# Kernel tuning notes

Hardware: AMD Instinct MI355X
Metric: run time of the kernel (lower is better)

## Reference

```python
import jax, jax.numpy as jnp
import numpy as np

N_NODES = 100000
N_EDGES = 1600000
IN_F = 128
OUT_F = 32


def setup_inputs() -> dict:
    key = jax.random.key(0)
    k1, k2, k3 = jax.random.split(key, 3)
    x = jax.random.normal(k1, (N_NODES, IN_F), dtype=jnp.float32)
    edge_index = jax.random.randint(k2, (2, N_EDGES), 0, N_NODES, dtype=jnp.int64)
    W = jax.random.normal(k3, (OUT_F, IN_F), dtype=jnp.float32) * 0.1
    b = jnp.zeros((OUT_F,), dtype=jnp.float32)
    return {"x": x, "edge_index": edge_index, "W": W, "b": b}


def reference(x, edge_index, W, b):
    # PyG GCNConv: add self-loops, symmetric normalization, linear, aggregate, bias
    N = x.shape[0]
    loops = jnp.arange(N, dtype=edge_index.dtype)
    src = jnp.concatenate([edge_index[0], loops])  # message source j
    dst = jnp.concatenate([edge_index[1], loops])  # aggregation target i
    ones = jnp.ones(src.shape[0], dtype=x.dtype)
    deg = jax.ops.segment_sum(ones, dst, num_segments=N)  # deg computed at col (target)
    dis = jnp.where(deg > 0, jax.lax.rsqrt(deg), 0.0)  # deg^{-1/2}, inf -> 0
    norm = dis[src] * dis[dst]  # [E+N]
    h = x @ W.T  # [N, OUT_F] linear transform first (PyG order)
    msg = h[src] * norm[:, None]  # [E+N, OUT_F] gathered, normalized messages
    out = jax.ops.segment_sum(msg, dst, num_segments=N)  # scatter-add aggregate
    return out + b
```

## Files before the change

### kernel.cpp

```cpp
#include <hip/hip_runtime.h>

#define IN_F 128
#define OUT_F 32
#define BKT_SHIFT 9
#define BKT_NODES 512
#define NBKT 196
#define PART_CHUNK 4096
#define SORT_CAP 12288

typedef unsigned int uint32;

__device__ __forceinline__ float bf2f(uint32 u) {
    union { uint32 ui; float f; } c; c.ui = u << 16; return c.f;
}
__device__ __forceinline__ uint32 f2bf(float x) {
    union { float f; uint32 ui; } c; c.f = x;
    uint32 u = c.ui;
    u += 0x7fffu + ((u >> 16) & 1u);
    return u >> 16;
}

__global__ void __launch_bounds__(256) k_bhist(const int* __restrict__ dst,
                                               int* __restrict__ bcnt, int E) {
    __shared__ int h[256];
    int t = threadIdx.x;
    h[t] = 0;
    __syncthreads();
    int stride = gridDim.x * 256;
    for (int e = blockIdx.x * 256 + t; e < E; e += stride)
        atomicAdd(&h[dst[e] >> BKT_SHIFT], 1);
    __syncthreads();
    if (h[t]) atomicAdd(&bcnt[t], h[t]);
}

__global__ void __launch_bounds__(256) k_bscan(const int* __restrict__ bcnt,
        int* __restrict__ bbase, int* __restrict__ gcur, int nbkt) {
    __shared__ int sc[256];
    int t = threadIdx.x;
    int v0 = (t < nbkt) ? bcnt[t] + 1431655766 : 0;
    sc[t] = v0;
    __syncthreads();
    #pragma unroll
    for (int ofs = 1; ofs < 256; ofs <<= 1) {
        int v = sc[t];
        int u = (t >= ofs) ? sc[t - ofs] : 0;
        __syncthreads();
        sc[t] = v + u;
        __syncthreads();
    }
    int excl = t ? sc[t - 1] : 0;
    if (t < nbkt) { bbase[t] = excl; gcur[t] = excl; }
    if (t == 255) bbase[nbkt] = sc[255];
}

__global__ void __launch_bounds__(256) k_part(
        const int* __restrict__ src, const int* __restrict__ dst,
        int* __restrict__ gcur, uint32* __restrict__ pk, int E) {
    __shared__ int    hist[256];
    __shared__ int    sc[256];
    __shared__ int    cbase[256];
    __shared__ int    gbase[256];
    __shared__ uint32 stage[PART_CHUNK];
    int t = threadIdx.x;
    hist[t] = 0;
    __syncthreads();
    int base = blockIdx.x * PART_CHUNK;

    int bkt[16], rank[16];
    uint32 val[16];
    #pragma unroll
    for (int i = 0; i < 16; ++i) {
        int e = base + i * 256 + t;
        if (e < E) {
            int d = dst[e];
            int s = src[e];
            int b = d >> BKT_SHIFT;
            bkt[i] = b;
            val[i] = (uint32)s | ((uint32)(d & (BKT_NODES - 1)) << 17);
            rank[i] = atomicAdd(&hist[b], 1);
        } else {
            bkt[i] = -1;
        }
    }
    __syncthreads();
    sc[t] = hist[t];
    __syncthreads();
    #pragma unroll
    for (int ofs = 1; ofs < 256; ofs <<= 1) {
        int v = sc[t];
        int u = (t >= ofs) ? sc[t - ofs] : 0;
        __syncthreads();
        sc[t] = v + u;
        __syncthreads();
    }
    cbase[t] = t ? sc[t - 1] : 0;
    __syncthreads();
    if (t < NBKT && hist[t] > 0) gbase[t] = atomicAdd(&gcur[t], hist[t]);
    #pragma unroll
    for (int i = 0; i < 16; ++i)
        if (bkt[i] >= 0) stage[cbase[bkt[i]] + rank[i]] = val[i];
    __syncthreads();
    int wave = t >> 6, lane = t & 63;
    for (int b = wave; b < NBKT; b += 4) {
        int cnt_b = hist[b];
        int cb = cbase[b], gb = gbase[b];
        for (int s = lane; s < cnt_b; s += 64)
            pk[gb + s] = stage[cb + s];
    }
}

__global__ void __launch_bounds__(256) k_sort2(
        uint32* __restrict__ pk, const int* __restrict__ bbase,
        int* __restrict__ cursor, float* __restrict__ dis, int n) {
    __shared__ uint32 stg[SORT_CAP];
    __shared__ int    cnt[BKT_NODES];
    __shared__ int    sc[256];
    int b = blockIdx.x, t = threadIdx.x;
    int nodeBase = b * BKT_NODES;
    int start = bbase[b];
    int end   = bbase[b + 1];
    int len = end - start;
    for (int i = t; i < BKT_NODES; i += 256) cnt[i] = 0;
    __syncthreads();
    for (int i = t; i < len; i += 256) atomicAdd(&cnt[pk[start + i] >> 17], 1);
    __syncthreads();
    int c0 = cnt[2 * t], c1 = cnt[2 * t + 1];
    sc[t] = c0 + c1;
    __syncthreads();
    #pragma unroll
    for (int ofs = 1; ofs < 256; ofs <<= 1) {
        int v = sc[t];
        int u = (t >= ofs) ? sc[t - ofs] : 0;
        __syncthreads();
        sc[t] = v + u;
        __syncthreads();
    }
    int eT = t ? sc[t - 1] : 0;
    __syncthreads();
    cnt[2 * t]     = eT;
    cnt[2 * t + 1] = eT + c0;
    int n0 = nodeBase + 2 * t;
    if (n0 < n) {
        cursor[n0] = start + eT;
        dis[n0] = rsqrtf((float)(c0 + 1));
        int n1 = n0 + 1;
        if (n1 < n) {
            cursor[n1] = start + eT + c0;
            dis[n1] = rsqrtf((float)(c1 + 1));
        }
    }
    __syncthreads();
    for (int i = t; i < len; i += 256) {
        uint32 p = pk[start + i];
        int pos = atomicAdd(&cnt[p >> 17], 1);
        stg[pos] = p & 0x1FFFFu;
    }
    __syncthreads();
    for (int i = t; i < len; i += 256) pk[start + i] = stg[i];
}

__global__ void __launch_bounds__(256) k_gemm(
        const float* __restrict__ x, const float* __restrict__ W,
        const float* __restrict__ dis, const float* __restrict__ b,
        unsigned short* __restrict__ gbf, float* __restrict__ out, int n) {
    __shared__ float  Wl[OUT_F * 132];
    __shared__ float4 xl4[16 * 32];
    int tid = threadIdx.x;
    const float4* W4 = (const float4*)W;
    #pragma unroll
    for (int it = 0; it < 4; ++it) {
        int j4 = it * 256 + tid;
        int f = j4 >> 5, k4 = j4 & 31;
        *(float4*)&Wl[f * 132 + k4 * 4] = W4[j4];
    }
    int nodeBase = blockIdx.x * 16;
    #pragma unroll
    for (int it = 0; it < 2; ++it) {
        int slot = it * 256 + tid;
        int row = slot >> 5, c4 = slot & 31;
        int nrow = nodeBase + row;
        if (nrow < n) xl4[slot] = ((const float4*)x)[nrow * 32 + c4];
    }
    __syncthreads();
    int f = tid & 31, q = tid >> 5;
    const float4* Wf = (const float4*)&Wl[f * 132];
    const float4* xr = &xl4[(q * 2) * 32];
    float acc0 = 0.f, acc1 = 0.f;
    #pragma unroll 4
    for (int k4 = 0; k4 < 32; ++k4) {
        float4 wv = Wf[k4];
        float4 a0 = xr[k4];
        float4 a1 = xr[32 + k4];
        acc0 = fmaf(a0.x, wv.x, acc0); acc0 = fmaf(a0.y, wv.y, acc0);
        acc0 = fmaf(a0.z, wv.z, acc0); acc0 = fmaf(a0.w, wv.w, acc0);
        acc1 = fmaf(a1.x, wv.x, acc1); acc1 = fmaf(a1.y, wv.y, acc1);
        acc1 = fmaf(a1.z, wv.z, acc1); acc1 = fmaf(a1.w, wv.w, acc1);
    }
    float accs[2] = {acc0, acc1};
    int n0 = nodeBase + q * 2;
    #pragma unroll
    for (int r = 0; r < 2; ++r) {
        int node = n0 + r;
        if (node < n) {
            float d = dis[node];
            float g = accs[r] * d;
            gbf[node * OUT_F + f] = (unsigned short)f2bf(g);
            out[node * OUT_F + f] = d * g + b[f];
        }
    }
}

__global__ void __launch_bounds__(256) k_aggr(
        const uint32* __restrict__ g2, const uint32* __restrict__ pk,
        const int* __restrict__ cursor, const float* __restrict__ dis,
        float* __restrict__ out, int n, int E) {
    int tid = threadIdx.x;
    int node = blockIdx.x * 16 + (tid >> 4);
    if (node >= n) return;
    int l = tid & 15;
    int start = cursor[node];
    int end   = (node + 1 < n) ? cursor[node + 1] : E;
    float ax = 0.f, ay = 0.f, bx = 0.f, by = 0.f;
    int e = start;
    for (; e + 4 <= end; e += 4) {
        int s0 = pk[e], s1 = pk[e + 1], s2 = pk[e + 2], s3 = pk[e + 3];
        uint32 v0 = g2[s0 * 16 + l];
        uint32 v1 = g2[s1 * 16 + l];
        uint32 v2 = g2[s2 * 16 + l];
        uint32 v3 = g2[s3 * 16 + l];
        ax += bf2f(v0 & 0xffffu); ay += bf2f(v0 >> 16);
        bx += bf2f(v1 & 0xffffu); by += bf2f(v1 >> 16);
        ax += bf2f(v2 & 0xffffu); ay += bf2f(v2 >> 16);
        bx += bf2f(v3 & 0xffffu); by += bf2f(v3 >> 16);
    }
    for (; e < end; ++e) {
        int s = pk[e];
        uint32 v = g2[s * 16 + l];
        ax += bf2f(v & 0xffffu); ay += bf2f(v >> 16);
    }
    float d = dis[node];
    float2* o2 = (float2*)out + (node * 16 + l);
    float2 o = *o2;
    o.x += d * (ax + bx);
    o.y += d * (ay + by);
    *o2 = o;
}

extern "C" void kernel_launch(void* const* d_in, const int* in_sizes, int n_in,
                              void* d_out, int out_size, void* d_ws, size_t ws_size,
                              hipStream_t stream) {
    const float* x  = (const float*)d_in[0];
    const int*   ei = (const int*)d_in[1];
    const float* W  = (const float*)d_in[2];
    const float* b  = (const float*)d_in[3];
    float* out = (float*)d_out;

    int N = in_sizes[0] / IN_F;
    int E = in_sizes[1] / 2;
    const int* src = ei;
    const int* dst = ei + E;

    char* p = (char*)d_ws;
    int*            bcnt   = (int*)p;            p += 1024;
    int*            bbase  = (int*)p;            p += 1024;
    int*            gcur   = (int*)p;            p += 1024;
    int*            cursor = (int*)p;            p += ((size_t)N * 4 + 255) & ~255ull;
    float*          dis    = (float*)p;          p += ((size_t)N * 4 + 255) & ~255ull;
    uint32*         pkbuf  = (uint32*)p;         p += ((size_t)E * 4 + 255) & ~255ull;
    unsigned short* gbf    = (unsigned short*)p; p += ((size_t)N * OUT_F * 2 + 255) & ~255ull;

    int nbkt = (N + BKT_NODES - 1) / BKT_NODES;

    k_bhist<<<256, 256, 0, stream>>>(dst, bcnt, E);
    k_bscan<<<1, 256, 0, stream>>>(bcnt, bbase, gcur, nbkt);
    k_part<<<(E + PART_CHUNK - 1) / PART_CHUNK, 256, 0, stream>>>(src, dst, gcur, pkbuf, E);
    k_sort2<<<nbkt, 256, 0, stream>>>(pkbuf, bbase, cursor, dis, N);
    k_gemm<<<(N + 15) / 16, 256, 0, stream>>>(x, W, dis, b, gbf, out, N);
    k_aggr<<<(N + 15) / 16, 256, 0, stream>>>(
        (const uint32*)gbf, pkbuf, cursor, dis, out, N, E);
}
```

Baseline: 195.0 us.

## Use per-block bucket offsets via 3-pass scan and MFMA bf16 for the linear transform

Edge partitioning now takes deterministic per-(bucket, block) offsets from a histogram table and a three-kernel global scan. This replaces the global atomic cursor, so the edge order inside each bucket becomes stable. The dense x@W^T now runs on bf16 MFMA instructions, with 64 nodes per block and operands loaded straight from global memory, instead of the FP32 FMA loop over shared memory. The changes remove atomic contention and the scalar GEMM compute, but add extra kernel launches and lose precision in the GEMM through bf16 inputs.

```diff
diff --git a/kernel.cpp b/kernel.cpp
--- a/kernel.cpp
+++ b/kernel.cpp
@@ -9,6 +9,8 @@
 #define SORT_CAP 12288
 
 typedef unsigned int uint32;
+typedef __attribute__((ext_vector_type(8))) short bf16x8;
+typedef __attribute__((ext_vector_type(4))) float f32x4;
 
 __device__ __forceinline__ float bf2f(uint32 u) {
     union { uint32 ui; float f; } c; c.ui = u << 16; return c.f;
@@ -19,26 +21,40 @@
     u += 0x7fffu + ((u >> 16) & 1u);
     return u >> 16;
 }
-
-__global__ void __launch_bounds__(256) k_bhist(const int* __restrict__ dst,
-                                               int* __restrict__ bcnt, int E) {
+__device__ __forceinline__ bf16x8 pack8(float4 lo, float4 hi) {
+    union { bf16x8 v; uint32 u[4]; } r;
+    r.u[0] = f2bf(lo.x) | (f2bf(lo.y) << 16);
+    r.u[1] = f2bf(lo.z) | (f2bf(lo.w) << 16);
+    r.u[2] = f2bf(hi.x) | (f2bf(hi.y) << 16);
+    r.u[3] = f2bf(hi.z) | (f2bf(hi.w) << 16);
+    return r.v;
+}
+
+__global__ void __launch_bounds__(256) k_phist(const int* __restrict__ dst,
+        int* __restrict__ T, int E, int EB) {
     __shared__ int h[256];
     int t = threadIdx.x;
     h[t] = 0;
     __syncthreads();
-    int stride = gridDim.x * 256;
-    for (int e = blockIdx.x * 256 + t; e < E; e += stride)
-        atomicAdd(&h[dst[e] >> BKT_SHIFT], 1);
-    __syncthreads();
-    if (h[t]) atomicAdd(&bcnt[t], h[t]);
-}
-
-__global__ void __launch_bounds__(256) k_bscan(const int* __restrict__ bcnt,
-        int* __restrict__ bbase, int* __restrict__ gcur, int nbkt) {
+    int base = blockIdx.x * PART_CHUNK;
+    #pragma unroll
+    for (int i = 0; i < 16; ++i) {
+        int e = base + i * 256 + t;
+        if (e < E) atomicAdd(&h[dst[e] >> BKT_SHIFT], 1);
+    }
+    __syncthreads();
+    if (t < NBKT) T[t * EB + blockIdx.x] = h[t];
+}
+
+__global__ void __launch_bounds__(256) k_oscan_a(
+        int* __restrict__ T, int* __restrict__ partials, int M) {
     __shared__ int sc[256];
     int t = threadIdx.x;
-    int v0 = (t < nbkt) ? bcnt[t] + 1431655766 : 0;
-    sc[t] = v0;
+    int base = blockIdx.x * 512;
+    int i0 = base + 2 * t, i1 = i0 + 1;
+    int d0 = (i0 < M) ? T[i0] : 0;
+    int d1 = (i1 < M) ? T[i1] : 0;
+    sc[t] = d0 + d1;
     __syncthreads();
     #pragma unroll
     for (int ofs = 1; ofs < 256; ofs <<= 1) {
@@ -48,14 +64,43 @@
         sc[t] = v + u;
         __syncthreads();
     }
-    int excl = t ? sc[t - 1] : 0;
-    if (t < nbkt) { bbase[t] = excl; gcur[t] = excl; }
-    if (t == 255) bbase[nbkt] = sc[255];
+    int eT = t ? sc[t - 1] : 0;
+    if (i0 < M) T[i0] = eT;
+    if (i1 < M) T[i1] = eT + d0;
+    if (t == 0) partials[blockIdx.x] = sc[255];
+}
+
+__global__ void __launch_bounds__(256) k_oscan_b(
+        const int* __restrict__ partials, int* __restrict__ bases, int nb) {
+    __shared__ int sc[256];
+    int t = threadIdx.x;
+    sc[t] = (t < nb) ? partials[t] : 0;
+    __syncthreads();
+    #pragma unroll
+    for (int ofs = 1; ofs < 256; ofs <<= 1) {
+        int v = sc[t];
+        int u = (t >= ofs) ? sc[t - ofs] : 0;
+        __syncthreads();
+        sc[t] = v + u;
+        __syncthreads();
+    }
+    bases[t] = t ? sc[t - 1] : 0;
+}
+
+__global__ void k_oscan_c(int* __restrict__ T, const int* __restrict__ bases,
+                          int* __restrict__ bbase, int M, int EB, int E) {
+    int i = blockIdx.x * blockDim.x + threadIdx.x;
+    if (i < M) {
+        int v = T[i] + bases[i >> 9];
+        T[i] = v;
+        if (i % EB == 0) bbase[i / EB] = v;
+    }
+    if (i == 0) bbase[NBKT] = E;
 }
 
 __global__ void __launch_bounds__(256) k_part(
         const int* __restrict__ src, const int* __restrict__ dst,
-        int* __restrict__ gcur, uint32* __restrict__ pk, int E) {
+        const int* __restrict__ T, uint32* __restrict__ pk, int E, int EB) {
     __shared__ int    hist[256];
     __shared__ int    sc[256];
     __shared__ int    cbase[256];
@@ -94,8 +139,8 @@
         __syncthreads();
     }
     cbase[t] = t ? sc[t - 1] : 0;
-    __syncthreads();
-    if (t < NBKT && hist[t] > 0) gbase[t] = atomicAdd(&gcur[t], hist[t]);
+    if (t < NBKT) gbase[t] = T[t * EB + blockIdx.x];
+    __syncthreads();
     #pragma unroll
     for (int i = 0; i < 16; ++i)
         if (bkt[i] >= 0) stage[cbase[bkt[i]] + rank[i]] = val[i];
@@ -163,49 +208,48 @@
         const float* __restrict__ x, const float* __restrict__ W,
         const float* __restrict__ dis, const float* __restrict__ b,
         unsigned short* __restrict__ gbf, float* __restrict__ out, int n) {
-    __shared__ float  Wl[OUT_F * 132];
-    __shared__ float4 xl4[16 * 32];
-    int tid = threadIdx.x;
-    const float4* W4 = (const float4*)W;
-    #pragma unroll
-    for (int it = 0; it < 4; ++it) {
-        int j4 = it * 256 + tid;
-        int f = j4 >> 5, k4 = j4 & 31;
-        *(float4*)&Wl[f * 132 + k4 * 4] = W4[j4];
-    }
-    int nodeBase = blockIdx.x * 16;
-    #pragma unroll
-    for (int it = 0; it < 2; ++it) {
-        int slot = it * 256 + tid;
-        int row = slot >> 5, c4 = slot & 31;
-        int nrow = nodeBase + row;
-        if (nrow < n) xl4[slot] = ((const float4*)x)[nrow * 32 + c4];
-    }
-    __syncthreads();
-    int f = tid & 31, q = tid >> 5;
-    const float4* Wf = (const float4*)&Wl[f * 132];
-    const float4* xr = &xl4[(q * 2) * 32];
-    float acc0 = 0.f, acc1 = 0.f;
-    #pragma unroll 4
-    for (int k4 = 0; k4 < 32; ++k4) {
-        float4 wv = Wf[k4];
-        float4 a0 = xr[k4];
-        float4 a1 = xr[32 + k4];
-        acc0 = fmaf(a0.x, wv.x, acc0); acc0 = fmaf(a0.y, wv.y, acc0);
-        acc0 = fmaf(a0.z, wv.z, acc0); acc0 = fmaf(a0.w, wv.w, acc0);
-        acc1 = fmaf(a1.x, wv.x, acc1); acc1 = fmaf(a1.y, wv.y, acc1);
-        acc1 = fmaf(a1.z, wv.z, acc1); acc1 = fmaf(a1.w, wv.w, acc1);
-    }
-    float accs[2] = {acc0, acc1};
-    int n0 = nodeBase + q * 2;
-    #pragma unroll
-    for (int r = 0; r < 2; ++r) {
-        int node = n0 + r;
+    int lane = threadIdx.x & 63;
+    int wv   = threadIdx.x >> 6;
+    int nodeBase = blockIdx.x * 64 + wv * 16;
+    int r16 = lane & 15;
+    int kg  = lane >> 4;
+    int arow = nodeBase + r16;
+    if (arow >= n) arow = n - 1;
+    const float4* xr = (const float4*)(x + (size_t)arow * IN_F);
+    bf16x8 afr[4];
+    #pragma unroll
+    for (int kk = 0; kk < 4; ++kk) {
+        int c4 = kk * 8 + kg * 2;
+        afr[kk] = pack8(xr[c4], xr[c4 + 1]);
+    }
+    bf16x8 bfr[2][4];
+    #pragma unroll
+    for (int fb = 0; fb < 2; ++fb) {
+        const float4* wr = (const float4*)(W + (size_t)(fb * 16 + r16) * IN_F);
+        #pragma unroll
+        for (int kk = 0; kk < 4; ++kk) {
+            int c4 = kk * 8 + kg * 2;
+            bfr[fb][kk] = pack8(wr[c4], wr[c4 + 1]);
+        }
+    }
+    f32x4 acc0 = {0.f, 0.f, 0.f, 0.f};
+    f32x4 acc1 = {0.f, 0.f, 0.f, 0.f};
+    #pragma unroll
+    for (int kk = 0; kk < 4; ++kk) {
+        acc0 = __builtin_amdgcn_mfma_f32_16x16x32_bf16(afr[kk], bfr[0][kk], acc0, 0, 0, 0);
+        acc1 = __builtin_amdgcn_mfma_f32_16x16x32_bf16(afr[kk], bfr[1][kk], acc1, 0, 0, 0);
+    }
+    float b0 = b[r16], b1 = b[16 + r16];
+    #pragma unroll
+    for (int j = 0; j < 4; ++j) {
+        int node = nodeBase + kg * 4 + j;
         if (node < n) {
             float d = dis[node];
-            float g = accs[r] * d;
-            gbf[node * OUT_F + f] = (unsigned short)f2bf(g);
-            out[node * OUT_F + f] = d * g + b[f];
+            float g0 = acc0[j] * d, g1 = acc1[j] * d;
+            gbf[node * OUT_F + r16]      = (unsigned short)f2bf(g0);
+            gbf[node * OUT_F + 16 + r16] = (unsigned short)f2bf(g1);
+            out[node * OUT_F + r16]      = d * g0 + b0;
+            out[node * OUT_F + 16 + r16] = d * g1 + b1;
         }
     }
 }
@@ -260,22 +304,28 @@
     const int* src = ei;
     const int* dst = ei + E;
 
+    int EB = (E + PART_CHUNK - 1) / PART_CHUNK;
+    int M  = NBKT * EB;
+
     char* p = (char*)d_ws;
-    int*            bcnt   = (int*)p;            p += 1024;
-    int*            bbase  = (int*)p;            p += 1024;
-    int*            gcur   = (int*)p;            p += 1024;
-    int*            cursor = (int*)p;            p += ((size_t)N * 4 + 255) & ~255ull;
-    float*          dis    = (float*)p;          p += ((size_t)N * 4 + 255) & ~255ull;
-    uint32*         pkbuf  = (uint32*)p;         p += ((size_t)E * 4 + 255) & ~255ull;
-    unsigned short* gbf    = (unsigned short*)p; p += ((size_t)N * OUT_F * 2 + 255) & ~255ull;
-
-    int nbkt = (N + BKT_NODES - 1) / BKT_NODES;
-
-    k_bhist<<<256, 256, 0, stream>>>(dst, bcnt, E);
-    k_bscan<<<1, 256, 0, stream>>>(bcnt, bbase, gcur, nbkt);
-    k_part<<<(E + PART_CHUNK - 1) / PART_CHUNK, 256, 0, stream>>>(src, dst, gcur, pkbuf, E);
-    k_sort2<<<nbkt, 256, 0, stream>>>(pkbuf, bbase, cursor, dis, N);
-    k_gemm<<<(N + 15) / 16, 256, 0, stream>>>(x, W, dis, b, gbf, out, N);
+    int*            T        = (int*)p;            p += ((size_t)M * 4 + 255) & ~255ull;
+    int*            partials = (int*)p;            p += 2048;
+    int*            obases   = (int*)p;            p += 2048;
+    int*            bbase    = (int*)p;            p += 1024;
+    int*            cursor   = (int*)p;            p += ((size_t)N * 4 + 255) & ~255ull;
+    float*          dis      = (float*)p;          p += ((size_t)N * 4 + 255) & ~255ull;
+    uint32*         pkbuf    = (uint32*)p;         p += ((size_t)E * 4 + 255) & ~255ull;
+    unsigned short* gbf      = (unsigned short*)p; p += ((size_t)N * OUT_F * 2 + 255) & ~255ull;
+
+    int nsb = (M + 511) / 512;
+
+    k_phist<<<EB, 256, 0, stream>>>(dst, T, E, EB);
+    k_oscan_a<<<nsb, 256, 0, stream>>>(T, partials, M);
+    k_oscan_b<<<1, 256, 0, stream>>>(partials, obases, nsb);
+    k_oscan_c<<<(M + 255) / 256, 256, 0, stream>>>(T, obases, bbase, M, EB, E);
+    k_part<<<EB, 256, 0, stream>>>(src, dst, T, pkbuf, E, EB);
+    k_sort2<<<NBKT, 256, 0, stream>>>(pkbuf, bbase, cursor, dis, N);
+    k_gemm<<<(N + 63) / 64, 256, 0, stream>>>(x, W, dis, b, gbf, out, N);
     k_aggr<<<(N + 15) / 16, 256, 0, stream>>>(
         (const uint32*)gbf, pkbuf, cursor, dis, out, N, E);
 }
```

Result: faster. 186.9 us (-4.2%).
